# Kernel tuning notes

Hardware: AMD Instinct MI355X
Metric: run time of the kernel (lower is better)

## Reference

```python
import jax, jax.numpy as jnp
import numpy as np

B, T, D, H = 4, 2048, 512, 8
SCALE = np.float32(1.0 / np.sqrt(D))  # 'vaswani' scale, tied scalar, non-trainable
MASK_BIAS = np.float32(1e9)           # TF dense_attention masking constant


def setup_inputs() -> dict:
    key = jax.random.key(0)
    ks = jax.random.split(key, 5)
    s = 0.02  # small init so softmax logits are well-scaled
    return {
        "query": jax.random.normal(ks[0], (B, T, D), jnp.float32),
        "value": jax.random.normal(ks[1], (B, T, D), jnp.float32),
        "Wq": jax.random.normal(ks[2], (D, D * H), jnp.float32) * s,
        "bq": jnp.zeros((D * H,), jnp.float32),
        "Wk": jax.random.normal(ks[3], (D, D * H), jnp.float32) * s,
        "bk": jnp.zeros((D * H,), jnp.float32),
        "Wv": jax.random.normal(ks[4], (D, D * H), jnp.float32) * s,
        "bv": jnp.zeros((D * H,), jnp.float32),
    }


def reference(query, value, Wq, bq, Wk, bk, Wv, bv):
    # Per-head Dense projections (linear activation, depth=1): [B,T,D] -> [B,T,H*D]
    # split(axis=-1) into H heads + concat(axis=0) == reshape to [B,T,H,D]
    # (head h occupies contiguous slice [h*D:(h+1)*D] of the last axis)
    q = (query @ Wq + bq).reshape(B, T, H, D)
    k = (value @ Wk + bk).reshape(B, T, H, D)  # key defaults to value
    v = (value @ Wv + bv).reshape(B, T, H, D)
    # multiplicative scores: matmul(scale*q, k^T) -> [B,H,Tq,Tv]
    scores = jnp.einsum('bqhd,bkhd->bhqk', SCALE * q, k)
    # causal mask applied TF-style: scores -= 1e9 * (~mask)
    causal = jnp.tril(jnp.ones((T, T), bool))
    scores = jnp.where(causal, scores, scores - MASK_BIAS)
    attn = jax.nn.softmax(scores, axis=-1)          # [B,H,Tq,Tv]
    out = jnp.einsum('bhqk,bkhd->bqhd', attn, v)    # [B,Tq,H,D]
    # heads_output_mode='cat': concat heads back on feature axis
    return out.reshape(B, T, H * D)
```

## Files before the change

kernel.cpp:

```cpp
#include <hip/hip_runtime.h>
#include <stdint.h>

#define Bsz 4
#define Tsz 2048
#define Dsz 512
#define Hsz 8
#define HDsz 4096
#define Msz 8192
#define SCALE 0.044194173824159216f

typedef __attribute__((ext_vector_type(8))) short bf16x8;
typedef __attribute__((ext_vector_type(4))) float f32x4;
typedef __attribute__((ext_vector_type(4))) short s16x4;

static __device__ __forceinline__ short f2bf(float x) {
    uint32_t b = __float_as_uint(x);
    b += 0x7fff + ((b >> 16) & 1);
    return (short)(b >> 16);
}

__global__ __launch_bounds__(256) void wtrans_kernel(
    const float* __restrict__ Wq, const float* __restrict__ Wk,
    const float* __restrict__ Wv, short* __restrict__ WtAll)
{
    const float* W = (blockIdx.z == 0) ? Wq : (blockIdx.z == 1) ? Wk : Wv;
    short* Wt = WtAll + (size_t)blockIdx.z * (size_t)HDsz * Dsz;
    __shared__ float tile[32][33];
    int tx = threadIdx.x, ty = threadIdx.y;
    int k0 = blockIdx.x * 32, n0 = blockIdx.y * 32;
    for (int i = 0; i < 4; i++)
        tile[ty + i * 8][tx] = W[(size_t)(k0 + ty + i * 8) * HDsz + n0 + tx];
    __syncthreads();
    for (int i = 0; i < 4; i++)
        Wt[(size_t)(n0 + ty + i * 8) * Dsz + k0 + tx] = f2bf(tile[tx][ty + i * 8]);
}

__global__ __launch_bounds__(256, 2) void proj_gemm_kernel(
    const float* __restrict__ Xq, const float* __restrict__ Xv,
    const short* __restrict__ WtAll, const float* __restrict__ bq,
    const float* __restrict__ bk, const float* __restrict__ bv,
    short* __restrict__ Qo, short* __restrict__ Ko, short* __restrict__ Vto)
{
    const int mode = blockIdx.z;
    const float* X = (mode == 0) ? Xq : Xv;
    const short* Wt = WtAll + (size_t)mode * (size_t)HDsz * Dsz;
    const float* bias = (mode == 0) ? bq : (mode == 1) ? bk : bv;
    const int m0 = blockIdx.x * 128, n0 = blockIdx.y * 128;

    __shared__ short Als[128 * 40];
    __shared__ short Bls[128 * 40];

    const int tid = threadIdx.x;
    const int lane = tid & 63, wave = tid >> 6;
    const int quad = lane >> 4, l16 = lane & 15;
    const int wm = wave >> 1, wn = wave & 1;

    f32x4 acc[4][4];
    for (int i = 0; i < 4; i++)
        for (int j = 0; j < 4; j++)
            acc[i][j] = f32x4{0.f, 0.f, 0.f, 0.f};

    for (int ks = 0; ks < Dsz; ks += 32) {
        __syncthreads();
        for (int p = 0; p < 4; p++) {
            int c = tid + p * 256;
            int row = c >> 3, ch = c & 7;
            float4 v = *(const float4*)&X[(size_t)(m0 + row) * Dsz + ks + ch * 4];
            s16x4 o;
            o.x = f2bf(v.x); o.y = f2bf(v.y); o.z = f2bf(v.z); o.w = f2bf(v.w);
            *(s16x4*)&Als[row * 40 + ch * 4] = o;
        }
        for (int p = 0; p < 2; p++) {
            int c = tid + p * 256;
            int row = c >> 2, ch = c & 3;
            *(bf16x8*)&Bls[row * 40 + ch * 8] =
                *(const bf16x8*)&Wt[(size_t)(n0 + row) * Dsz + ks + ch * 8];
        }
        __syncthreads();
        bf16x8 af[4], bfr[4];
        for (int i = 0; i < 4; i++)
            af[i] = *(const bf16x8*)&Als[(wm * 64 + i * 16 + l16) * 40 + quad * 8];
        for (int j = 0; j < 4; j++)
            bfr[j] = *(const bf16x8*)&Bls[(wn * 64 + j * 16 + l16) * 40 + quad * 8];
        for (int i = 0; i < 4; i++)
            for (int j = 0; j < 4; j++)
                acc[i][j] = __builtin_amdgcn_mfma_f32_16x16x32_bf16(
                    af[i], bfr[j], acc[i][j], 0, 0, 0);
    }

    for (int i = 0; i < 4; i++) {
        for (int j = 0; j < 4; j++) {
            int n = n0 + wn * 64 + j * 16 + l16;
            int h = n >> 9, d = n & 511;
            float bb = bias[n];
            int mbase = m0 + wm * 64 + i * 16 + quad * 4;
            int b = mbase >> 11, t = mbase & 2047;
            if (mode == 2) {
                s16x4 o;
                o.x = f2bf(acc[i][j][0] + bb);
                o.y = f2bf(acc[i][j][1] + bb);
                o.z = f2bf(acc[i][j][2] + bb);
                o.w = f2bf(acc[i][j][3] + bb);
                *(s16x4*)&Vto[((size_t)(b * Hsz + h) * Dsz + d) * Tsz + t] = o;
            } else {
                short* O = (mode == 0) ? Qo : Ko;
                float sc = (mode == 0) ? SCALE : 1.0f;
                for (int r = 0; r < 4; r++) {
                    float v = (acc[i][j][r] + bb) * sc;
                    O[((size_t)(b * Hsz + h) * Tsz + (t + r)) * Dsz + d] = f2bf(v);
                }
            }
        }
    }
}

__global__ __launch_bounds__(512, 2) void attn_kernel(
    const short* __restrict__ Q, const short* __restrict__ K,
    const short* __restrict__ Vt, float* __restrict__ out)
{
    extern __shared__ short smem[];
    short* Ks  = smem;
    short* Vs  = smem + 64 * 520;
    short* Pls = Vs + 512 * 72;

    const int bid = blockIdx.x;
    const int qt = 15 - (bid >> 5);
    const int bh = bid & 31;
    const int q0 = qt * 128;

    const short* Qb = Q + (size_t)bh * Tsz * Dsz;
    const short* Kb = K + (size_t)bh * Tsz * Dsz;
    const short* Vb = Vt + (size_t)bh * Dsz * Tsz;

    const int tid = threadIdx.x;
    const int lane = tid & 63, wave = tid >> 6;
    const int quad = lane >> 4, l16 = lane & 15;
    const int qw = q0 + wave * 16;
    short* Pw = Pls + wave * (16 * 72);

    bf16x8 qf[16];
    for (int ks = 0; ks < 16; ks++)
        qf[ks] = *(const bf16x8*)&Qb[(size_t)(qw + l16) * Dsz + ks * 32 + quad * 8];

    f32x4 acc[32];
    for (int dt = 0; dt < 32; dt++) acc[dt] = f32x4{0.f, 0.f, 0.f, 0.f};
    float lacc[4] = {0.f, 0.f, 0.f, 0.f};

    const int nkv = 2 * (qt + 1);
    for (int kt = 0; kt < nkv; kt++) {
        const int kv0 = kt * 64;

        bf16x8 vtmp[8];
        for (int p = 0; p < 8; p++) {
            int c = p * 512 + tid;
            vtmp[p] = *(const bf16x8*)&Vb[(size_t)(c >> 3) * Tsz + kv0 + (c & 7) * 8];
        }
        __syncthreads();
        for (int p = 0; p < 8; p++) {
            int c = p * 512 + tid;
            *(bf16x8*)&Vs[(c >> 3) * 72 + (c & 7) * 8] = vtmp[p];
        }
        for (int i = 0; i < 8; i++) {
            int r = wave * 8 + i;
            const short* gp = Kb + (size_t)(kv0 + r) * Dsz + lane * 8;
            __builtin_amdgcn_global_load_lds(
                (const __attribute__((address_space(1))) void*)gp,
                (__attribute__((address_space(3))) void*)&Ks[r * 520], 16, 0, 0);
        }
        __syncthreads();

        if (kv0 <= qw + 15) {
            f32x4 s[4];
            for (int j = 0; j < 4; j++) s[j] = f32x4{0.f, 0.f, 0.f, 0.f};
            for (int ks = 0; ks < 16; ks++)
                for (int j = 0; j < 4; j++) {
                    bf16x8 kb = *(const bf16x8*)&Ks[(j * 16 + l16) * 520 + ks * 32 + quad * 8];
                    s[j] = __builtin_amdgcn_mfma_f32_16x16x32_bf16(qf[ks], kb, s[j], 0, 0, 0);
                }

            bool full = (kv0 + 63 <= qw);
            for (int r = 0; r < 4; r++) {
                int rowg = qw + quad * 4 + r;
                for (int j = 0; j < 4; j++) {
                    float p = __expf(fminf(s[j][r], 40.f));
                    if (!full && (kv0 + j * 16 + l16 > rowg)) p = 0.f;
                    lacc[r] += p;
                    Pw[(quad * 4 + r) * 72 + j * 16 + l16] = f2bf(p);
                }
            }

            bf16x8 pa0 = *(const bf16x8*)&Pw[l16 * 72 + quad * 8];
            bf16x8 pa1 = *(const bf16x8*)&Pw[l16 * 72 + 32 + quad * 8];
            for (int dt = 0; dt < 32; dt++) {
                bf16x8 vb0 = *(const bf16x8*)&Vs[(dt * 16 + l16) * 72 + quad * 8];
                bf16x8 vb1 = *(const bf16x8*)&Vs[(dt * 16 + l16) * 72 + 32 + quad * 8];
                acc[dt] = __builtin_amdgcn_mfma_f32_16x16x32_bf16(pa0, vb0, acc[dt], 0, 0, 0);
                acc[dt] = __builtin_amdgcn_mfma_f32_16x16x32_bf16(pa1, vb1, acc[dt], 0, 0, 0);
            }
        }
    }

    const int b = bh >> 3, h = bh & 7;
    float inv[4];
    for (int r = 0; r < 4; r++) {
        float l = lacc[r];
        l += __shfl_xor(l, 1);
        l += __shfl_xor(l, 2);
        l += __shfl_xor(l, 4);
        l += __shfl_xor(l, 8);
        inv[r] = 1.0f / l;
    }
    for (int dt = 0; dt < 32; dt++) {
        for (int r = 0; r < 4; r++) {
            int t = qw + quad * 4 + r;
            out[(size_t)(b * Tsz + t) * HDsz + h * Dsz + dt * 16 + l16] =
                acc[dt][r] * inv[r];
        }
    }
}

extern "C" void kernel_launch(void* const* d_in, const int* in_sizes, int n_in,
                              void* d_out, int out_size, void* d_ws, size_t ws_size,
                              hipStream_t stream) {
    const float* query = (const float*)d_in[0];
    const float* value = (const float*)d_in[1];
    const float* Wq = (const float*)d_in[2];
    const float* bq = (const float*)d_in[3];
    const float* Wk = (const float*)d_in[4];
    const float* bk = (const float*)d_in[5];
    const float* Wv = (const float*)d_in[6];
    const float* bv = (const float*)d_in[7];
    float* out = (float*)d_out;

    char* ws = (char*)d_ws;
    short* Wt  = (short*)ws;
    short* Qb  = (short*)(ws + 12582912);
    short* Kb  = (short*)(ws + 12582912 + 67108864);
    short* Vtb = (short*)(ws + 12582912 + 2 * 67108864);

    hipFuncSetAttribute((const void*)attn_kernel,
                        hipFuncAttributeMaxDynamicSharedMemorySize, 158720);

    wtrans_kernel<<<dim3(16, 128, 3), dim3(32, 8), 0, stream>>>(Wq, Wk, Wv, Wt);
    proj_gemm_kernel<<<dim3(64, 32, 3), 256, 0, stream>>>(
        query, value, Wt, bq, bk, bv, Qb, Kb, Vtb);
    attn_kernel<<<dim3(512), dim3(512), 158720, stream>>>(Qb, Kb, Vtb, out);
}
```

Before: 591.1 us.

## Pre-cast inputs to bf16, DMA GEMM tiles to LDS, double-buffer attention KV

Adds a separate kernel that casts query and value to bf16 once, so the projection GEMM can stage its A and B tiles with direct global-to-LDS loads into an XOR-swizzled, unpadded layout instead of converting in registers. The attention kernel moves to 32-wide KV tiles with double-buffered K/V LDS. The next tile's K is prefetched through async LDS loads and its V through registers while the current tile is computed, leaving one barrier per iteration. This costs an extra launch and an extra bf16 copy of the inputs in memory, and uses smaller MFMA batches per tile.

```diff
diff --git a/kernel.cpp b/kernel.cpp
--- a/kernel.cpp
+++ b/kernel.cpp
@@ -17,6 +17,20 @@
     uint32_t b = __float_as_uint(x);
     b += 0x7fff + ((b >> 16) & 1);
     return (short)(b >> 16);
+}
+
+__global__ __launch_bounds__(256) void xcast_kernel(
+    const float* __restrict__ Xq, const float* __restrict__ Xv,
+    short* __restrict__ Oq, short* __restrict__ Ov)
+{
+    int idx = blockIdx.x * 256 + threadIdx.x;
+    const float* src = (idx < 1048576) ? Xq : Xv;
+    short* dst = (idx < 1048576) ? Oq : Ov;
+    int i = (idx < 1048576) ? idx : idx - 1048576;
+    float4 v = *(const float4*)&src[(size_t)i * 4];
+    s16x4 o;
+    o.x = f2bf(v.x); o.y = f2bf(v.y); o.z = f2bf(v.z); o.w = f2bf(v.w);
+    *(s16x4*)&dst[(size_t)i * 4] = o;
 }
 
 __global__ __launch_bounds__(256) void wtrans_kernel(
@@ -36,25 +50,29 @@
 }
 
 __global__ __launch_bounds__(256, 2) void proj_gemm_kernel(
-    const float* __restrict__ Xq, const float* __restrict__ Xv,
+    const short* __restrict__ Xqb, const short* __restrict__ Xvb,
     const short* __restrict__ WtAll, const float* __restrict__ bq,
     const float* __restrict__ bk, const float* __restrict__ bv,
     short* __restrict__ Qo, short* __restrict__ Ko, short* __restrict__ Vto)
 {
     const int mode = blockIdx.z;
-    const float* X = (mode == 0) ? Xq : Xv;
+    const short* X = (mode == 0) ? Xqb : Xvb;
     const short* Wt = WtAll + (size_t)mode * (size_t)HDsz * Dsz;
     const float* bias = (mode == 0) ? bq : (mode == 1) ? bk : bv;
     const int m0 = blockIdx.x * 128, n0 = blockIdx.y * 128;
 
-    __shared__ short Als[128 * 40];
-    __shared__ short Bls[128 * 40];
+    __shared__ short Als[128 * 32];
+    __shared__ short Bls[128 * 32];
 
     const int tid = threadIdx.x;
     const int lane = tid & 63, wave = tid >> 6;
     const int quad = lane >> 4, l16 = lane & 15;
     const int wm = wave >> 1, wn = wave & 1;
 
+    const int dmarow = lane >> 2;
+    const int dmachunk = (lane & 3) ^ ((lane >> 3) & 3);
+    const int rdsw = (quad ^ ((l16 >> 1) & 3)) * 8;
+
     f32x4 acc[4][4];
     for (int i = 0; i < 4; i++)
         for (int j = 0; j < 4; j++)
@@ -62,26 +80,24 @@
 
     for (int ks = 0; ks < Dsz; ks += 32) {
         __syncthreads();
-        for (int p = 0; p < 4; p++) {
-            int c = tid + p * 256;
-            int row = c >> 3, ch = c & 7;
-            float4 v = *(const float4*)&X[(size_t)(m0 + row) * Dsz + ks + ch * 4];
-            s16x4 o;
-            o.x = f2bf(v.x); o.y = f2bf(v.y); o.z = f2bf(v.z); o.w = f2bf(v.w);
-            *(s16x4*)&Als[row * 40 + ch * 4] = o;
-        }
-        for (int p = 0; p < 2; p++) {
-            int c = tid + p * 256;
-            int row = c >> 2, ch = c & 3;
-            *(bf16x8*)&Bls[row * 40 + ch * 8] =
-                *(const bf16x8*)&Wt[(size_t)(n0 + row) * Dsz + ks + ch * 8];
+        for (int s = 0; s < 2; s++) {
+            int c = wave * 2 + s;
+            int row = c * 16 + dmarow;
+            const short* ga = X + (size_t)(m0 + row) * Dsz + ks + dmachunk * 8;
+            __builtin_amdgcn_global_load_lds(
+                (const __attribute__((address_space(1))) void*)ga,
+                (__attribute__((address_space(3))) void*)&Als[c * 512], 16, 0, 0);
+            const short* gb = Wt + (size_t)(n0 + row) * Dsz + ks + dmachunk * 8;
+            __builtin_amdgcn_global_load_lds(
+                (const __attribute__((address_space(1))) void*)gb,
+                (__attribute__((address_space(3))) void*)&Bls[c * 512], 16, 0, 0);
         }
         __syncthreads();
         bf16x8 af[4], bfr[4];
         for (int i = 0; i < 4; i++)
-            af[i] = *(const bf16x8*)&Als[(wm * 64 + i * 16 + l16) * 40 + quad * 8];
+            af[i] = *(const bf16x8*)&Als[(wm * 64 + i * 16 + l16) * 32 + rdsw];
         for (int j = 0; j < 4; j++)
-            bfr[j] = *(const bf16x8*)&Bls[(wn * 64 + j * 16 + l16) * 40 + quad * 8];
+            bfr[j] = *(const bf16x8*)&Bls[(wn * 64 + j * 16 + l16) * 32 + rdsw];
         for (int i = 0; i < 4; i++)
             for (int j = 0; j < 4; j++)
                 acc[i][j] = __builtin_amdgcn_mfma_f32_16x16x32_bf16(
@@ -119,15 +135,11 @@
     const short* __restrict__ Vt, float* __restrict__ out)
 {
     extern __shared__ short smem[];
-    short* Ks  = smem;
-    short* Vs  = smem + 64 * 520;
-    short* Pls = Vs + 512 * 72;
 
     const int bid = blockIdx.x;
     const int qt = 15 - (bid >> 5);
     const int bh = bid & 31;
     const int q0 = qt * 128;
-
     const short* Qb = Q + (size_t)bh * Tsz * Dsz;
     const short* Kb = K + (size_t)bh * Tsz * Dsz;
     const short* Vb = Vt + (size_t)bh * Dsz * Tsz;
@@ -136,7 +148,8 @@
     const int lane = tid & 63, wave = tid >> 6;
     const int quad = lane >> 4, l16 = lane & 15;
     const int qw = q0 + wave * 16;
-    short* Pw = Pls + wave * (16 * 72);
+    short* Pw = smem + 74240 + wave * (16 * 40);
+    const int vrow = tid >> 2, vch = tid & 3;
 
     bf16x8 qf[16];
     for (int ks = 0; ks < 16; ks++)
@@ -146,58 +159,84 @@
     for (int dt = 0; dt < 32; dt++) acc[dt] = f32x4{0.f, 0.f, 0.f, 0.f};
     float lacc[4] = {0.f, 0.f, 0.f, 0.f};
 
-    const int nkv = 2 * (qt + 1);
-    for (int kt = 0; kt < nkv; kt++) {
-        const int kv0 = kt * 64;
-
-        bf16x8 vtmp[8];
-        for (int p = 0; p < 8; p++) {
-            int c = p * 512 + tid;
-            vtmp[p] = *(const bf16x8*)&Vb[(size_t)(c >> 3) * Tsz + kv0 + (c & 7) * 8];
-        }
-        __syncthreads();
-        for (int p = 0; p < 8; p++) {
-            int c = p * 512 + tid;
-            *(bf16x8*)&Vs[(c >> 3) * 72 + (c & 7) * 8] = vtmp[p];
-        }
-        for (int i = 0; i < 8; i++) {
-            int r = wave * 8 + i;
-            const short* gp = Kb + (size_t)(kv0 + r) * Dsz + lane * 8;
+    {
+        short* Ks0 = smem;
+        short* Vs0 = smem + 33280;
+        for (int i = 0; i < 4; i++) {
+            int r = wave * 4 + i;
+            const short* gp = Kb + (size_t)r * Dsz + lane * 8;
             __builtin_amdgcn_global_load_lds(
                 (const __attribute__((address_space(1))) void*)gp,
-                (__attribute__((address_space(3))) void*)&Ks[r * 520], 16, 0, 0);
-        }
-        __syncthreads();
+                (__attribute__((address_space(3))) void*)&Ks0[r * 520], 16, 0, 0);
+        }
+        for (int p = 0; p < 4; p++) {
+            int row = p * 128 + vrow;
+            bf16x8 v = *(const bf16x8*)&Vb[(size_t)row * Tsz + vch * 8];
+            *(bf16x8*)&Vs0[row * 40 + vch * 8] = v;
+        }
+    }
+    __syncthreads();
+
+    const int nkv = 4 * (qt + 1);
+    for (int kt = 0; kt < nkv; kt++) {
+        const int kv0 = kt * 32;
+        short* Ksc = smem + (kt & 1) * 16640;
+        short* Vsc = smem + 33280 + (kt & 1) * 20480;
+        const bool pref = (kt + 1 < nkv);
+
+        bf16x8 vreg[4];
+        if (pref) {
+            const int kvn = kv0 + 32;
+            short* Ksn = smem + ((kt + 1) & 1) * 16640;
+            for (int i = 0; i < 4; i++) {
+                int r = wave * 4 + i;
+                const short* gp = Kb + (size_t)(kvn + r) * Dsz + lane * 8;
+                __builtin_amdgcn_global_load_lds(
+                    (const __attribute__((address_space(1))) void*)gp,
+                    (__attribute__((address_space(3))) void*)&Ksn[r * 520], 16, 0, 0);
+            }
+            for (int p = 0; p < 4; p++) {
+                int row = p * 128 + vrow;
+                vreg[p] = *(const bf16x8*)&Vb[(size_t)row * Tsz + kvn + vch * 8];
+            }
+        }
 
         if (kv0 <= qw + 15) {
-            f32x4 s[4];
-            for (int j = 0; j < 4; j++) s[j] = f32x4{0.f, 0.f, 0.f, 0.f};
-            for (int ks = 0; ks < 16; ks++)
-                for (int j = 0; j < 4; j++) {
-                    bf16x8 kb = *(const bf16x8*)&Ks[(j * 16 + l16) * 520 + ks * 32 + quad * 8];
-                    s[j] = __builtin_amdgcn_mfma_f32_16x16x32_bf16(qf[ks], kb, s[j], 0, 0, 0);
-                }
-
-            bool full = (kv0 + 63 <= qw);
+            f32x4 s0 = f32x4{0.f, 0.f, 0.f, 0.f}, s1 = f32x4{0.f, 0.f, 0.f, 0.f};
+            for (int ks = 0; ks < 16; ks++) {
+                bf16x8 b0 = *(const bf16x8*)&Ksc[l16 * 520 + ks * 32 + quad * 8];
+                bf16x8 b1 = *(const bf16x8*)&Ksc[(16 + l16) * 520 + ks * 32 + quad * 8];
+                s0 = __builtin_amdgcn_mfma_f32_16x16x32_bf16(qf[ks], b0, s0, 0, 0, 0);
+                s1 = __builtin_amdgcn_mfma_f32_16x16x32_bf16(qf[ks], b1, s1, 0, 0, 0);
+            }
+            bool full = (kv0 + 31 <= qw);
             for (int r = 0; r < 4; r++) {
                 int rowg = qw + quad * 4 + r;
-                for (int j = 0; j < 4; j++) {
-                    float p = __expf(fminf(s[j][r], 40.f));
-                    if (!full && (kv0 + j * 16 + l16 > rowg)) p = 0.f;
-                    lacc[r] += p;
-                    Pw[(quad * 4 + r) * 72 + j * 16 + l16] = f2bf(p);
+                float p0 = __expf(fminf(s0[r], 40.f));
+                float p1 = __expf(fminf(s1[r], 40.f));
+                if (!full) {
+                    if (kv0 + l16 > rowg) p0 = 0.f;
+                    if (kv0 + 16 + l16 > rowg) p1 = 0.f;
                 }
-            }
-
-            bf16x8 pa0 = *(const bf16x8*)&Pw[l16 * 72 + quad * 8];
-            bf16x8 pa1 = *(const bf16x8*)&Pw[l16 * 72 + 32 + quad * 8];
+                lacc[r] += p0 + p1;
+                Pw[(quad * 4 + r) * 40 + l16] = f2bf(p0);
+                Pw[(quad * 4 + r) * 40 + 16 + l16] = f2bf(p1);
+            }
+            bf16x8 pa = *(const bf16x8*)&Pw[l16 * 40 + quad * 8];
             for (int dt = 0; dt < 32; dt++) {
-                bf16x8 vb0 = *(const bf16x8*)&Vs[(dt * 16 + l16) * 72 + quad * 8];
-                bf16x8 vb1 = *(const bf16x8*)&Vs[(dt * 16 + l16) * 72 + 32 + quad * 8];
-                acc[dt] = __builtin_amdgcn_mfma_f32_16x16x32_bf16(pa0, vb0, acc[dt], 0, 0, 0);
-                acc[dt] = __builtin_amdgcn_mfma_f32_16x16x32_bf16(pa1, vb1, acc[dt], 0, 0, 0);
-            }
-        }
+                bf16x8 vb = *(const bf16x8*)&Vsc[(dt * 16 + l16) * 40 + quad * 8];
+                acc[dt] = __builtin_amdgcn_mfma_f32_16x16x32_bf16(pa, vb, acc[dt], 0, 0, 0);
+            }
+        }
+
+        if (pref) {
+            short* Vsn = smem + 33280 + ((kt + 1) & 1) * 20480;
+            for (int p = 0; p < 4; p++) {
+                int row = p * 128 + vrow;
+                *(bf16x8*)&Vsn[row * 40 + vch * 8] = vreg[p];
+            }
+        }
+        __syncthreads();
     }
 
     const int b = bh >> 3, h = bh & 7;
@@ -234,15 +273,18 @@
 
     char* ws = (char*)d_ws;
     short* Wt  = (short*)ws;
-    short* Qb  = (short*)(ws + 12582912);
-    short* Kb  = (short*)(ws + 12582912 + 67108864);
-    short* Vtb = (short*)(ws + 12582912 + 2 * 67108864);
-
-    hipFuncSetAttribute((const void*)attn_kernel,
+    short* Xqb = (short*)(ws + 12582912);
+    short* Xvb = (short*)(ws + 20971520);
+    short* Qb  = (short*)(ws + 29360128);
+    short* Kb  = (short*)(ws + 96468992);
+    short* Vtb = (short*)(ws + 163577856);
+
+    (void)hipFuncSetAttribute((const void*)attn_kernel,
                         hipFuncAttributeMaxDynamicSharedMemorySize, 158720);
 
+    xcast_kernel<<<8192, 256, 0, stream>>>(query, value, Xqb, Xvb);
     wtrans_kernel<<<dim3(16, 128, 3), dim3(32, 8), 0, stream>>>(Wq, Wk, Wv, Wt);
     proj_gemm_kernel<<<dim3(64, 32, 3), 256, 0, stream>>>(
-        query, value, Wt, bq, bk, bv, Qb, Kb, Vtb);
+        Xqb, Xvb, Wt, bq, bk, bv, Qb, Kb, Vtb);
     attn_kernel<<<dim3(512), dim3(512), 158720, stream>>>(Qb, Kb, Vtb, out);
 }
```

Measured after the change: 550.2 us. 1.07x faster.
